# Kernel optimization log

Hardware: AMD Instinct MI355X
Metric: run time of the kernel (lower is better)

## Reference

```python
import jax, jax.numpy as jnp
import numpy as np

D_MODEL = 512
DFF = 2048
E = 8
K = 2
B, N = 2, 2048


def setup_inputs() -> dict:
    key = jax.random.key(0)
    ks = jax.random.split(key, 6)
    x = jax.random.normal(ks[0], (B, N, D_MODEL), dtype=jnp.float32)
    # router: nn.Linear(d_model, E, bias=False), init normal(std=0.01), weight [E, d]
    router_w = jax.random.normal(ks[1], (E, D_MODEL), dtype=jnp.float32) * 0.01
    # expert linear1.weight [dff, d], linear2.weight [d, dff], xavier-uniform; biases zero in torch init,
    # but use small random biases so the backward test exercises their grads meaningfully.
    lim1 = float(np.sqrt(6.0 / (D_MODEL + DFF)))
    w1_all = jax.random.uniform(ks[2], (E, DFF, D_MODEL), minval=-lim1, maxval=lim1, dtype=jnp.float32)
    w2_all = jax.random.uniform(ks[3], (E, D_MODEL, DFF), minval=-lim1, maxval=lim1, dtype=jnp.float32)
    b1_all = jax.random.normal(ks[4], (E, DFF), dtype=jnp.float32) * 0.01
    b2_all = jax.random.normal(ks[5], (E, D_MODEL), dtype=jnp.float32) * 0.01
    return {"x": x, "router_w": router_w, "w1_all": w1_all, "b1_all": b1_all,
            "w2_all": w2_all, "b2_all": b2_all}


def reference(x, router_w, w1_all, b1_all, w2_all, b2_all):
    Bb, Nn, C = x.shape
    L = Bb * Nn
    x_flat = x.reshape(L, C)

    # Router: logits -> softmax -> top-k -> renormalized weights
    router_logits = x_flat @ router_w.T                      # [L, E]
    router_probs = jax.nn.softmax(router_logits, axis=-1)
    expert_weights, expert_indices = jax.lax.top_k(router_probs, K)  # [L, K]
    expert_weights = expert_weights / (jnp.sum(expert_weights, axis=-1, keepdims=True) + 1e-9)

    # Dense per-expert MLP (same math as per-token gathered bmm; dropout in eval = identity)
    h = jax.nn.relu(jnp.einsum('lc,efc->lef', x_flat, w1_all) + b1_all[None])  # [L, E, dff]
    out_all = jnp.einsum('lef,ecf->lec', h, w2_all) + b2_all[None]             # [L, E, C]

    # Gather selected experts' outputs and combine
    out_sel = jnp.take_along_axis(out_all, expert_indices[:, :, None], axis=1)  # [L, K, C]
    final = jnp.sum(out_sel * expert_weights[:, :, None], axis=1)               # [L, C]
    return final.reshape(Bb, Nn, C)
```

## Files before the change

### kernel.cpp

```cpp
#include <hip/hip_runtime.h>

#define D_MODEL 512
#define DFF 2048
#define NEXP 8
#define LTOK 4096
#define NPAIR 8192
#define PMAX 9216
#define MAXT 72

#define HD_COUNTS 0
#define HD_CURSOR 8
#define HD_OFF    16
#define HD_NTILES 25
#define HD_TILE_E 32
#define HD_TILE_R 112

typedef __attribute__((ext_vector_type(8))) short bf16x8;
typedef __attribute__((ext_vector_type(4))) float f32x4;

__device__ __forceinline__ unsigned short f2bf(float f){
  unsigned u = __builtin_bit_cast(unsigned, f);
  u += 0x7fffu + ((u>>16)&1u);
  return (unsigned short)(u>>16);
}

__global__ void router_top2(const float* __restrict__ x, const float* __restrict__ rw,
                            int* __restrict__ pair_e, float* __restrict__ pair_w){
  int t = blockIdx.x;
  int l = threadIdx.x;
  const float* xr = x + (size_t)t*D_MODEL;
  float xv[8];
  #pragma unroll
  for (int j=0;j<8;j++) xv[j] = xr[j*64+l];
  double lg[NEXP];
  #pragma unroll
  for (int e=0;e<NEXP;e++){
    const float* we = rw + e*D_MODEL;
    double s = 0.0;
    #pragma unroll
    for (int j=0;j<8;j++) s += (double)xv[j] * (double)we[j*64+l];
    #pragma unroll
    for (int off=32; off; off>>=1) s += __shfl_xor(s, off);
    lg[e] = s;
  }
  if (l==0){
    double mx = lg[0];
    #pragma unroll
    for (int e=1;e<NEXP;e++) if (lg[e]>mx) mx = lg[e];
    double p[NEXP], sum = 0.0;
    #pragma unroll
    for (int e=0;e<NEXP;e++){ p[e] = exp(lg[e]-mx); sum += p[e]; }
    #pragma unroll
    for (int e=0;e<NEXP;e++) p[e] /= sum;
    int i0 = 0;
    for (int e=1;e<NEXP;e++) if (p[e] > p[i0]) i0 = e;
    int i1 = (i0==0) ? 1 : 0;
    for (int e=0;e<NEXP;e++){ if (e==i0) continue; if (p[e] > p[i1]) i1 = e; }
    double s2 = p[i0] + p[i1] + 1e-9;
    pair_e[2*t]   = i0;  pair_e[2*t+1] = i1;
    pair_w[2*t]   = (float)(p[i0]/s2);
    pair_w[2*t+1] = (float)(p[i1]/s2);
  }
}

__global__ void count_kernel(const int* __restrict__ pair_e, int* __restrict__ hdr){
  __shared__ int cnt[NEXP];
  int tid = threadIdx.x;
  if (tid < NEXP) cnt[tid] = 0;
  __syncthreads();
  int base = blockIdx.x*1024;
  #pragma unroll
  for (int i=0;i<4;i++) atomicAdd(&cnt[pair_e[base + i*256 + tid]], 1);
  __syncthreads();
  if (tid < NEXP) atomicAdd(&hdr[HD_COUNTS+tid], cnt[tid]);
}

__global__ void plan_kernel(int* __restrict__ hdr, int* __restrict__ gtok,
                            int* __restrict__ gtk){
  if (threadIdx.x==0){
    int off=0, nt=0;
    for (int e=0;e<NEXP;e++){
      hdr[HD_OFF+e]=off;
      int c = hdr[HD_COUNTS+e];
      int tiles = (c+127)>>7;
      for (int i=0;i<tiles;i++){ hdr[HD_TILE_E+nt]=e; hdr[HD_TILE_R+nt]=off+(i<<7); nt++; }
      off += tiles<<7;
    }
    hdr[HD_OFF+NEXP]=off;
    hdr[HD_NTILES]=nt;
  }
  for (int i=threadIdx.x; i<PMAX; i+=blockDim.x){ gtok[i]=0; gtk[i]=-1; }
}

__global__ void assign_kernel(const int* __restrict__ pair_e, int* __restrict__ hdr,
                              int* __restrict__ gtok, int* __restrict__ gtk){
  __shared__ int cnt[NEXP];
  __shared__ int base[NEXP];
  int tid = threadIdx.x;
  if (tid < NEXP) cnt[tid] = 0;
  __syncthreads();
  int id = blockIdx.x*256 + tid;
  int e = pair_e[id];
  int myrank = atomicAdd(&cnt[e], 1);
  __syncthreads();
  if (tid < NEXP) base[tid] = atomicAdd(&hdr[HD_CURSOR+tid], cnt[tid]);
  __syncthreads();
  int row = hdr[HD_OFF+e] + base[e] + myrank;
  gtok[row] = id>>1;
  gtk[row]  = id;
}

__global__ void gather_x_kernel(const float* __restrict__ x, const int* __restrict__ gtok,
                                unsigned short* __restrict__ xg){
  int id = blockIdx.x*256 + threadIdx.x;
  if (id >= PMAX*(D_MODEL/8)) return;
  int row = id>>6, j = id&63;
  int t = gtok[row];
  const float4* s = (const float4*)(x + (size_t)t*D_MODEL + j*8);
  float4 a = s[0], b = s[1];
  uint4 o;
  o.x = (unsigned)f2bf(a.x) | ((unsigned)f2bf(a.y)<<16);
  o.y = (unsigned)f2bf(a.z) | ((unsigned)f2bf(a.w)<<16);
  o.z = (unsigned)f2bf(b.x) | ((unsigned)f2bf(b.y)<<16);
  o.w = (unsigned)f2bf(b.z) | ((unsigned)f2bf(b.w)<<16);
  *(uint4*)(xg + (size_t)id*8) = o;
}

__global__ void convw_kernel(const float* __restrict__ w1, const float* __restrict__ w2,
                             unsigned short* __restrict__ w1b, unsigned short* __restrict__ w2b){
  int id = blockIdx.x*256 + threadIdx.x;
  const int per = NEXP*DFF*D_MODEL/8;
  const float* src; unsigned short* dst; int k;
  if (id < per){ src = w1; dst = w1b; k = id; }
  else         { src = w2; dst = w2b; k = id - per; }
  const float4* s = (const float4*)(src + (size_t)k*8);
  float4 a = s[0], b = s[1];
  uint4 o;
  o.x = (unsigned)f2bf(a.x) | ((unsigned)f2bf(a.y)<<16);
  o.y = (unsigned)f2bf(a.z) | ((unsigned)f2bf(a.w)<<16);
  o.z = (unsigned)f2bf(b.x) | ((unsigned)f2bf(b.y)<<16);
  o.w = (unsigned)f2bf(b.z) | ((unsigned)f2bf(b.w)<<16);
  *(uint4*)(dst + (size_t)k*8) = o;
}

template<int NDIM, int KDIM, int MODE>
__global__ __launch_bounds__(256,2) void gemm_moe(
    const unsigned short* __restrict__ A,
    const unsigned short* __restrict__ Bw,
    const float* __restrict__ bias,
    unsigned short* __restrict__ outH,
    float* __restrict__ outO,
    const float* __restrict__ pair_w,
    const int* __restrict__ hdr,
    const int* __restrict__ gtk)
{
  __shared__ __align__(16) unsigned short As[128*64];
  __shared__ __align__(16) unsigned short Bs[128*64];
  int bx = blockIdx.x;
  if (bx >= hdr[HD_NTILES]) return;
  int e    = hdr[HD_TILE_E+bx];
  int row0 = hdr[HD_TILE_R+bx];
  int n0   = blockIdx.y<<7;
  int tid  = threadIdx.x;
  int w = tid>>6, l = tid&63;
  int wm = w>>1, wn = w&1;

  const unsigned short* Ag = A  + (size_t)row0*KDIM;
  const unsigned short* Bg = Bw + (size_t)e*NDIM*KDIM + (size_t)n0*KDIM;

  f32x4 acc[4][4];
  f32x4 zz = {0.f,0.f,0.f,0.f};
  #pragma unroll
  for (int i=0;i<4;i++)
    #pragma unroll
    for (int j=0;j<4;j++) acc[i][j] = zz;

  int srow = (w<<3) + (l>>3);
  int c8   = l&7;
  char* AsB = (char*)As;
  char* BsB = (char*)Bs;

  for (int kt=0; kt<KDIM/64; ++kt){
    #pragma unroll
    for (int i=0;i<4;i++){
      int r  = i*32 + srow;
      int sc = (c8 ^ (r&7))*8;
      const unsigned short* ga = Ag + (size_t)r*KDIM + kt*64 + sc;
      const unsigned short* gb = Bg + (size_t)r*KDIM + kt*64 + sc;
      int ldso = i*4096 + w*1024 + l*16;
      __builtin_amdgcn_global_load_lds((const __attribute__((address_space(1))) void*)ga,
                                       (__attribute__((address_space(3))) void*)(AsB + ldso), 16, 0, 0);
      __builtin_amdgcn_global_load_lds((const __attribute__((address_space(1))) void*)gb,
                                       (__attribute__((address_space(3))) void*)(BsB + ldso), 16, 0, 0);
    }
    __syncthreads();
    #pragma unroll
    for (int kk=0;kk<2;kk++){
      bf16x8 av[4], bv[4];
      #pragma unroll
      for (int mi=0;mi<4;mi++){
        int r  = (wm<<6) + (mi<<4) + (l&15);
        int ch = ((kk<<2) + (l>>4)) ^ (r&7);
        av[mi] = *(const bf16x8*)(AsB + r*128 + ch*16);
      }
      #pragma unroll
      for (int ni=0;ni<4;ni++){
        int r  = (wn<<6) + (ni<<4) + (l&15);
        int ch = ((kk<<2) + (l>>4)) ^ (r&7);
        bv[ni] = *(const bf16x8*)(BsB + r*128 + ch*16);
      }
      #pragma unroll
      for (int mi=0;mi<4;mi++)
        #pragma unroll
        for (int ni=0;ni<4;ni++)
          acc[mi][ni] = __builtin_amdgcn_mfma_f32_16x16x32_bf16(av[mi], bv[ni], acc[mi][ni], 0,0,0);
    }
    __syncthreads();
  }

  int lc = l&15, lq = l>>4;
  #pragma unroll
  for (int ni=0;ni<4;ni++){
    int col = n0 + (wn<<6) + (ni<<4) + lc;
    float bcol = bias[e*NDIM + col];
    #pragma unroll
    for (int mi=0;mi<4;mi++){
      int rbase = row0 + (wm<<6) + (mi<<4) + lq*4;
      #pragma unroll
      for (int q=0;q<4;q++){
        int gr = rbase + q;
        float v = acc[mi][ni][q] + bcol;
        if (MODE==0){
          v = v>0.f ? v : 0.f;
          outH[(size_t)gr*NDIM + col] = f2bf(v);
        } else {
          int tk = gtk[gr];
          if (tk>=0){
            float wgt = pair_w[tk];
            atomicAdd(&outO[(size_t)(tk>>1)*D_MODEL + col], wgt*v);
          }
        }
      }
    }
  }
}

extern "C" void kernel_launch(void* const* d_in, const int* in_sizes, int n_in,
                              void* d_out, int out_size, void* d_ws, size_t ws_size,
                              hipStream_t stream){
  const float* x  = (const float*)d_in[0];
  const float* rw = (const float*)d_in[1];
  const float* w1 = (const float*)d_in[2];
  const float* b1 = (const float*)d_in[3];
  const float* w2 = (const float*)d_in[4];
  const float* b2 = (const float*)d_in[5];
  float* out = (float*)d_out;

  const size_t OFF_HDR  = 0;
  const size_t OFF_PE   = 1024;
  const size_t OFF_PW   = 66560;
  const size_t OFF_GTOK = 99328;
  const size_t OFF_GTK  = 136192;
  const size_t OFF_XG   = 180224;
  const size_t OFF_W1B  = OFF_XG  + (size_t)PMAX*D_MODEL*2;
  const size_t OFF_W2B  = OFF_W1B + (size_t)NEXP*DFF*D_MODEL*2;
  const size_t OFF_H    = OFF_W2B + (size_t)NEXP*DFF*D_MODEL*2;
  const size_t WS_NEED  = OFF_H   + (size_t)PMAX*DFF*2;
  if (ws_size < WS_NEED) return;

  char* ws = (char*)d_ws;
  int*   hdr    = (int*)(ws + OFF_HDR);
  int*   pair_e = (int*)(ws + OFF_PE);
  float* pair_w = (float*)(ws + OFF_PW);
  int*   gtok   = (int*)(ws + OFF_GTOK);
  int*   gtk    = (int*)(ws + OFF_GTK);
  unsigned short* xg  = (unsigned short*)(ws + OFF_XG);
  unsigned short* w1b = (unsigned short*)(ws + OFF_W1B);
  unsigned short* w2b = (unsigned short*)(ws + OFF_W2B);
  unsigned short* h   = (unsigned short*)(ws + OFF_H);

  hipMemsetAsync(hdr, 0, 1024, stream);
  hipMemsetAsync(out, 0, (size_t)LTOK*D_MODEL*sizeof(float), stream);
  router_top2<<<LTOK, 64, 0, stream>>>(x, rw, pair_e, pair_w);
  count_kernel<<<NPAIR/1024, 256, 0, stream>>>(pair_e, hdr);
  plan_kernel<<<1, 256, 0, stream>>>(hdr, gtok, gtk);
  assign_kernel<<<NPAIR/256, 256, 0, stream>>>(pair_e, hdr, gtok, gtk);
  gather_x_kernel<<<(PMAX*64)/256, 256, 0, stream>>>(x, gtok, xg);
  convw_kernel<<<8192, 256, 0, stream>>>(w1, w2, w1b, w2b);
  gemm_moe<DFF, D_MODEL, 0><<<dim3(MAXT,16), 256, 0, stream>>>(xg, w1b, b1, h, nullptr, nullptr, hdr, gtk);
  gemm_moe<D_MODEL, DFF, 1><<<dim3(MAXT,4), 256, 0, stream>>>(h, w2b, b2, nullptr, out, pair_w, hdr, gtk);
}
```

Before: 154.0 us.

## Fuse prep kernels and double-buffer both MoE GEMMs with retuned tiles

Merges weight conversion with the router, and merges token assignment with the x gather, which cuts kernel launches and the gtok buffer. Both expert GEMMs now use double-buffered LDS staging with async global-to-LDS loads, partial vmcnt waits and raw barriers, so loads overlap MFMA work. GEMM1 uses 128x256 tiles with 8 waves, GEMM2 uses 64x128 tiles with higher occupancy, and both use a workgroup swizzle for locality. The risks are correctness of the manual waitcnt and barrier handling, and padding rows of xg that are no longer zero-filled.

Result: no change. 156.8 us (+1.8%).

```diff
diff --git a/kernel.cpp b/kernel.cpp
--- a/kernel.cpp
+++ b/kernel.cpp
@@ -24,42 +24,68 @@
   return (unsigned short)(u>>16);
 }
 
-__global__ void router_top2(const float* __restrict__ x, const float* __restrict__ rw,
+template<int N> __device__ __forceinline__ void wait_vm(){
+  if constexpr (N==6)      asm volatile("s_waitcnt vmcnt(6)" ::: "memory");
+  else                     asm volatile("s_waitcnt vmcnt(0)" ::: "memory");
+}
+#define RAW_BARRIER() asm volatile("s_barrier" ::: "memory")
+
+__global__ void prep_kernel(const float* __restrict__ w1, const float* __restrict__ w2,
+                            unsigned short* __restrict__ w1b, unsigned short* __restrict__ w2b,
+                            const float* __restrict__ x, const float* __restrict__ rw,
                             int* __restrict__ pair_e, float* __restrict__ pair_w){
-  int t = blockIdx.x;
-  int l = threadIdx.x;
-  const float* xr = x + (size_t)t*D_MODEL;
-  float xv[8];
-  #pragma unroll
-  for (int j=0;j<8;j++) xv[j] = xr[j*64+l];
-  double lg[NEXP];
-  #pragma unroll
-  for (int e=0;e<NEXP;e++){
-    const float* we = rw + e*D_MODEL;
-    double s = 0.0;
-    #pragma unroll
-    for (int j=0;j<8;j++) s += (double)xv[j] * (double)we[j*64+l];
-    #pragma unroll
-    for (int off=32; off; off>>=1) s += __shfl_xor(s, off);
-    lg[e] = s;
-  }
-  if (l==0){
-    double mx = lg[0];
-    #pragma unroll
-    for (int e=1;e<NEXP;e++) if (lg[e]>mx) mx = lg[e];
-    double p[NEXP], sum = 0.0;
-    #pragma unroll
-    for (int e=0;e<NEXP;e++){ p[e] = exp(lg[e]-mx); sum += p[e]; }
-    #pragma unroll
-    for (int e=0;e<NEXP;e++) p[e] /= sum;
-    int i0 = 0;
-    for (int e=1;e<NEXP;e++) if (p[e] > p[i0]) i0 = e;
-    int i1 = (i0==0) ? 1 : 0;
-    for (int e=0;e<NEXP;e++){ if (e==i0) continue; if (p[e] > p[i1]) i1 = e; }
-    double s2 = p[i0] + p[i1] + 1e-9;
-    pair_e[2*t]   = i0;  pair_e[2*t+1] = i1;
-    pair_w[2*t]   = (float)(p[i0]/s2);
-    pair_w[2*t+1] = (float)(p[i1]/s2);
+  int bx = blockIdx.x;
+  int tid = threadIdx.x;
+  if (bx < 8192){
+    int id = bx*256 + tid;
+    const int per = NEXP*DFF*D_MODEL/8;
+    const float* src; unsigned short* dst; int k;
+    if (id < per){ src = w1; dst = w1b; k = id; }
+    else         { src = w2; dst = w2b; k = id - per; }
+    const float4* s = (const float4*)(src + (size_t)k*8);
+    float4 a = s[0], b = s[1];
+    uint4 o;
+    o.x = (unsigned)f2bf(a.x) | ((unsigned)f2bf(a.y)<<16);
+    o.y = (unsigned)f2bf(a.z) | ((unsigned)f2bf(a.w)<<16);
+    o.z = (unsigned)f2bf(b.x) | ((unsigned)f2bf(b.y)<<16);
+    o.w = (unsigned)f2bf(b.z) | ((unsigned)f2bf(b.w)<<16);
+    *(uint4*)(dst + (size_t)k*8) = o;
+  } else {
+    int t = (bx - 8192)*4 + (tid>>6);
+    int l = tid & 63;
+    const float* xr = x + (size_t)t*D_MODEL;
+    float xv[8];
+    #pragma unroll
+    for (int j=0;j<8;j++) xv[j] = xr[j*64+l];
+    double lg[NEXP];
+    #pragma unroll
+    for (int e=0;e<NEXP;e++){
+      const float* we = rw + e*D_MODEL;
+      double s = 0.0;
+      #pragma unroll
+      for (int j=0;j<8;j++) s += (double)xv[j] * (double)we[j*64+l];
+      #pragma unroll
+      for (int off=32; off; off>>=1) s += __shfl_xor(s, off);
+      lg[e] = s;
+    }
+    if (l==0){
+      double mx = lg[0];
+      #pragma unroll
+      for (int e=1;e<NEXP;e++) if (lg[e]>mx) mx = lg[e];
+      double p[NEXP], sum = 0.0;
+      #pragma unroll
+      for (int e=0;e<NEXP;e++){ p[e] = exp(lg[e]-mx); sum += p[e]; }
+      #pragma unroll
+      for (int e=0;e<NEXP;e++) p[e] /= sum;
+      int i0 = 0;
+      for (int e=1;e<NEXP;e++) if (p[e] > p[i0]) i0 = e;
+      int i1 = (i0==0) ? 1 : 0;
+      for (int e=0;e<NEXP;e++){ if (e==i0) continue; if (p[e] > p[i1]) i1 = e; }
+      double s2 = p[i0] + p[i1] + 1e-9;
+      pair_e[2*t]   = i0;  pair_e[2*t+1] = i1;
+      pair_w[2*t]   = (float)(p[i0]/s2);
+      pair_w[2*t+1] = (float)(p[i1]/s2);
+    }
   }
 }
 
@@ -75,8 +101,7 @@
   if (tid < NEXP) atomicAdd(&hdr[HD_COUNTS+tid], cnt[tid]);
 }
 
-__global__ void plan_kernel(int* __restrict__ hdr, int* __restrict__ gtok,
-                            int* __restrict__ gtk){
+__global__ void plan_kernel(int* __restrict__ hdr, int* __restrict__ gtk){
   if (threadIdx.x==0){
     int off=0, nt=0;
     for (int e=0;e<NEXP;e++){
@@ -89,13 +114,15 @@
     hdr[HD_OFF+NEXP]=off;
     hdr[HD_NTILES]=nt;
   }
-  for (int i=threadIdx.x; i<PMAX; i+=blockDim.x){ gtok[i]=0; gtk[i]=-1; }
-}
-
-__global__ void assign_kernel(const int* __restrict__ pair_e, int* __restrict__ hdr,
-                              int* __restrict__ gtok, int* __restrict__ gtk){
+  for (int i=threadIdx.x; i<PMAX; i+=blockDim.x) gtk[i]=-1;
+}
+
+__global__ void assign_gather_kernel(const int* __restrict__ pair_e, int* __restrict__ hdr,
+                                     int* __restrict__ gtk, const float* __restrict__ x,
+                                     unsigned short* __restrict__ xg){
   __shared__ int cnt[NEXP];
   __shared__ int base[NEXP];
+  __shared__ int rowbuf[256];
   int tid = threadIdx.x;
   if (tid < NEXP) cnt[tid] = 0;
   __syncthreads();
@@ -106,139 +133,258 @@
   if (tid < NEXP) base[tid] = atomicAdd(&hdr[HD_CURSOR+tid], cnt[tid]);
   __syncthreads();
   int row = hdr[HD_OFF+e] + base[e] + myrank;
-  gtok[row] = id>>1;
-  gtk[row]  = id;
-}
-
-__global__ void gather_x_kernel(const float* __restrict__ x, const int* __restrict__ gtok,
-                                unsigned short* __restrict__ xg){
-  int id = blockIdx.x*256 + threadIdx.x;
-  if (id >= PMAX*(D_MODEL/8)) return;
-  int row = id>>6, j = id&63;
-  int t = gtok[row];
-  const float4* s = (const float4*)(x + (size_t)t*D_MODEL + j*8);
-  float4 a = s[0], b = s[1];
-  uint4 o;
-  o.x = (unsigned)f2bf(a.x) | ((unsigned)f2bf(a.y)<<16);
-  o.y = (unsigned)f2bf(a.z) | ((unsigned)f2bf(a.w)<<16);
-  o.z = (unsigned)f2bf(b.x) | ((unsigned)f2bf(b.y)<<16);
-  o.w = (unsigned)f2bf(b.z) | ((unsigned)f2bf(b.w)<<16);
-  *(uint4*)(xg + (size_t)id*8) = o;
-}
-
-__global__ void convw_kernel(const float* __restrict__ w1, const float* __restrict__ w2,
-                             unsigned short* __restrict__ w1b, unsigned short* __restrict__ w2b){
-  int id = blockIdx.x*256 + threadIdx.x;
-  const int per = NEXP*DFF*D_MODEL/8;
-  const float* src; unsigned short* dst; int k;
-  if (id < per){ src = w1; dst = w1b; k = id; }
-  else         { src = w2; dst = w2b; k = id - per; }
-  const float4* s = (const float4*)(src + (size_t)k*8);
-  float4 a = s[0], b = s[1];
-  uint4 o;
-  o.x = (unsigned)f2bf(a.x) | ((unsigned)f2bf(a.y)<<16);
-  o.y = (unsigned)f2bf(a.z) | ((unsigned)f2bf(a.w)<<16);
-  o.z = (unsigned)f2bf(b.x) | ((unsigned)f2bf(b.y)<<16);
-  o.w = (unsigned)f2bf(b.z) | ((unsigned)f2bf(b.w)<<16);
-  *(uint4*)(dst + (size_t)k*8) = o;
-}
-
-template<int NDIM, int KDIM, int MODE>
-__global__ __launch_bounds__(256,2) void gemm_moe(
+  gtk[row] = id;
+  rowbuf[tid] = row;
+  __syncthreads();
+  int grp = tid>>6, sub = tid&63;
+  int base0 = blockIdx.x*256;
+  for (int p = grp; p < 256; p += 4){
+    int r = rowbuf[p];
+    int t = (base0 + p)>>1;
+    const float4* s = (const float4*)(x + (size_t)t*D_MODEL + sub*8);
+    float4 a = s[0], b = s[1];
+    uint4 o;
+    o.x = (unsigned)f2bf(a.x) | ((unsigned)f2bf(a.y)<<16);
+    o.y = (unsigned)f2bf(a.z) | ((unsigned)f2bf(a.w)<<16);
+    o.z = (unsigned)f2bf(b.x) | ((unsigned)f2bf(b.y)<<16);
+    o.w = (unsigned)f2bf(b.z) | ((unsigned)f2bf(b.w)<<16);
+    *(uint4*)(xg + (size_t)r*D_MODEL + sub*8) = o;
+  }
+}
+
+__global__ __launch_bounds__(512,2) void gemm1_k(
     const unsigned short* __restrict__ A,
     const unsigned short* __restrict__ Bw,
     const float* __restrict__ bias,
     unsigned short* __restrict__ outH,
+    const int* __restrict__ hdr)
+{
+  constexpr int NWG = MAXT*8;
+  __shared__ __align__(16) unsigned short As[2*128*64];
+  __shared__ __align__(16) unsigned short Bs[2*256*64];
+
+  int wg  = blockIdx.x;
+  int swz = (wg & 7)*(NWG/8) + (wg >> 3);
+  int m   = swz >> 3;
+  int n0  = (swz & 7) << 8;
+
+  if (m >= hdr[HD_NTILES]) return;
+  int e    = hdr[HD_TILE_E+m];
+  int row0 = hdr[HD_TILE_R+m];
+
+  int tid = threadIdx.x;
+  int w = tid>>6, l = tid&63;
+  int wm = w>>2, wn = w&3;
+
+  const unsigned short* Ag = A  + (size_t)row0*D_MODEL;
+  const unsigned short* Bg = Bw + (size_t)e*DFF*D_MODEL + (size_t)n0*D_MODEL;
+
+  f32x4 acc[4][4];
+  f32x4 zz = {0.f,0.f,0.f,0.f};
+  #pragma unroll
+  for (int i=0;i<4;i++)
+    #pragma unroll
+    for (int j=0;j<4;j++) acc[i][j] = zz;
+
+  int srow = (w<<3) + (l>>3);
+  int c8   = l&7;
+  char* AsB = (char*)As;
+  char* BsB = (char*)Bs;
+
+  auto stage = [&](int b, int kt){
+    #pragma unroll
+    for (int i=0;i<2;i++){
+      int r  = i*64 + srow;
+      int sc = (c8 ^ (r&7))*8;
+      const unsigned short* ga = Ag + (size_t)r*D_MODEL + kt*64 + sc;
+      int ldso = b*16384 + i*8192 + w*1024 + l*16;
+      __builtin_amdgcn_global_load_lds((const __attribute__((address_space(1))) void*)ga,
+                                       (__attribute__((address_space(3))) void*)(AsB + ldso), 16, 0, 0);
+    }
+    #pragma unroll
+    for (int i=0;i<4;i++){
+      int r  = i*64 + srow;
+      int sc = (c8 ^ (r&7))*8;
+      const unsigned short* gb = Bg + (size_t)r*D_MODEL + kt*64 + sc;
+      int ldso = b*32768 + i*8192 + w*1024 + l*16;
+      __builtin_amdgcn_global_load_lds((const __attribute__((address_space(1))) void*)gb,
+                                       (__attribute__((address_space(3))) void*)(BsB + ldso), 16, 0, 0);
+    }
+  };
+
+  auto compute = [&](int b){
+    #pragma unroll
+    for (int kk=0;kk<2;kk++){
+      bf16x8 av[4], bv[4];
+      #pragma unroll
+      for (int mi=0;mi<4;mi++){
+        int r  = (wm<<6) + (mi<<4) + (l&15);
+        int ch = ((kk<<2) + (l>>4)) ^ (r&7);
+        av[mi] = *(const bf16x8*)(AsB + b*16384 + r*128 + ch*16);
+      }
+      #pragma unroll
+      for (int ni=0;ni<4;ni++){
+        int r  = (wn<<6) + (ni<<4) + (l&15);
+        int ch = ((kk<<2) + (l>>4)) ^ (r&7);
+        bv[ni] = *(const bf16x8*)(BsB + b*32768 + r*128 + ch*16);
+      }
+      #pragma unroll
+      for (int mi=0;mi<4;mi++)
+        #pragma unroll
+        for (int ni=0;ni<4;ni++)
+          acc[mi][ni] = __builtin_amdgcn_mfma_f32_16x16x32_bf16(av[mi], bv[ni], acc[mi][ni], 0,0,0);
+    }
+  };
+
+  stage(0, 0);
+  int cur = 0;
+  for (int kt=0; kt<D_MODEL/64-1; ++kt){
+    stage(cur^1, kt+1);
+    wait_vm<6>();
+    RAW_BARRIER();
+    compute(cur);
+    asm volatile("s_waitcnt lgkmcnt(0)" ::: "memory");
+    RAW_BARRIER();
+    cur ^= 1;
+  }
+  wait_vm<0>();
+  RAW_BARRIER();
+  compute(cur);
+
+  int lc = l&15, lq = l>>4;
+  #pragma unroll
+  for (int ni=0;ni<4;ni++){
+    int col = n0 + (wn<<6) + (ni<<4) + lc;
+    float bcol = bias[e*DFF + col];
+    #pragma unroll
+    for (int mi=0;mi<4;mi++){
+      int rbase = row0 + (wm<<6) + (mi<<4) + lq*4;
+      #pragma unroll
+      for (int q=0;q<4;q++){
+        float v = acc[mi][ni][q] + bcol;
+        v = v>0.f ? v : 0.f;
+        outH[(size_t)(rbase+q)*DFF + col] = f2bf(v);
+      }
+    }
+  }
+}
+
+__global__ __launch_bounds__(256,3) void gemm2_k(
+    const unsigned short* __restrict__ A,
+    const unsigned short* __restrict__ Bw,
+    const float* __restrict__ bias,
     float* __restrict__ outO,
     const float* __restrict__ pair_w,
     const int* __restrict__ hdr,
     const int* __restrict__ gtk)
 {
-  __shared__ __align__(16) unsigned short As[128*64];
-  __shared__ __align__(16) unsigned short Bs[128*64];
-  int bx = blockIdx.x;
-  if (bx >= hdr[HD_NTILES]) return;
-  int e    = hdr[HD_TILE_E+bx];
-  int row0 = hdr[HD_TILE_R+bx];
-  int n0   = blockIdx.y<<7;
-  int tid  = threadIdx.x;
+  constexpr int NWG = 2*MAXT*4;
+  __shared__ __align__(16) unsigned short As[2*64*64];
+  __shared__ __align__(16) unsigned short Bs[2*128*64];
+
+  int wg  = blockIdx.x;
+  int swz = (wg & 7)*(NWG/8) + (wg >> 3);
+  int m   = swz >> 2;
+  int n0  = (swz & 3) << 7;
+
+  if (m >= 2*hdr[HD_NTILES]) return;
+  int e    = hdr[HD_TILE_E+(m>>1)];
+  int row0 = hdr[HD_TILE_R+(m>>1)] + ((m&1)<<6);
+
+  int tid = threadIdx.x;
   int w = tid>>6, l = tid&63;
-  int wm = w>>1, wn = w&1;
-
-  const unsigned short* Ag = A  + (size_t)row0*KDIM;
-  const unsigned short* Bg = Bw + (size_t)e*NDIM*KDIM + (size_t)n0*KDIM;
-
-  f32x4 acc[4][4];
+
+  const unsigned short* Ag = A  + (size_t)row0*DFF;
+  const unsigned short* Bg = Bw + (size_t)e*D_MODEL*DFF + (size_t)n0*DFF;
+
+  f32x4 acc[4][2];
   f32x4 zz = {0.f,0.f,0.f,0.f};
   #pragma unroll
   for (int i=0;i<4;i++)
     #pragma unroll
-    for (int j=0;j<4;j++) acc[i][j] = zz;
+    for (int j=0;j<2;j++) acc[i][j] = zz;
 
   int srow = (w<<3) + (l>>3);
   int c8   = l&7;
   char* AsB = (char*)As;
   char* BsB = (char*)Bs;
 
-  for (int kt=0; kt<KDIM/64; ++kt){
+  auto stage = [&](int b, int kt){
+    #pragma unroll
+    for (int i=0;i<2;i++){
+      int r  = i*32 + srow;
+      int sc = (c8 ^ (r&7))*8;
+      const unsigned short* ga = Ag + (size_t)r*DFF + kt*64 + sc;
+      int ldso = b*8192 + i*4096 + w*1024 + l*16;
+      __builtin_amdgcn_global_load_lds((const __attribute__((address_space(1))) void*)ga,
+                                       (__attribute__((address_space(3))) void*)(AsB + ldso), 16, 0, 0);
+    }
     #pragma unroll
     for (int i=0;i<4;i++){
       int r  = i*32 + srow;
       int sc = (c8 ^ (r&7))*8;
-      const unsigned short* ga = Ag + (size_t)r*KDIM + kt*64 + sc;
-      const unsigned short* gb = Bg + (size_t)r*KDIM + kt*64 + sc;
-      int ldso = i*4096 + w*1024 + l*16;
-      __builtin_amdgcn_global_load_lds((const __attribute__((address_space(1))) void*)ga,
-                                       (__attribute__((address_space(3))) void*)(AsB + ldso), 16, 0, 0);
+      const unsigned short* gb = Bg + (size_t)r*DFF + kt*64 + sc;
+      int ldso = b*16384 + i*4096 + w*1024 + l*16;
       __builtin_amdgcn_global_load_lds((const __attribute__((address_space(1))) void*)gb,
                                        (__attribute__((address_space(3))) void*)(BsB + ldso), 16, 0, 0);
     }
-    __syncthreads();
+  };
+
+  auto compute = [&](int b){
     #pragma unroll
     for (int kk=0;kk<2;kk++){
-      bf16x8 av[4], bv[4];
+      bf16x8 av[4], bv[2];
       #pragma unroll
       for (int mi=0;mi<4;mi++){
-        int r  = (wm<<6) + (mi<<4) + (l&15);
+        int r  = (mi<<4) + (l&15);
         int ch = ((kk<<2) + (l>>4)) ^ (r&7);
-        av[mi] = *(const bf16x8*)(AsB + r*128 + ch*16);
-      }
-      #pragma unroll
-      for (int ni=0;ni<4;ni++){
-        int r  = (wn<<6) + (ni<<4) + (l&15);
+        av[mi] = *(const bf16x8*)(AsB + b*8192 + r*128 + ch*16);
+      }
+      #pragma unroll
+      for (int ni=0;ni<2;ni++){
+        int r  = (w<<5) + (ni<<4) + (l&15);
         int ch = ((kk<<2) + (l>>4)) ^ (r&7);
-        bv[ni] = *(const bf16x8*)(BsB + r*128 + ch*16);
+        bv[ni] = *(const bf16x8*)(BsB + b*16384 + r*128 + ch*16);
       }
       #pragma unroll
       for (int mi=0;mi<4;mi++)
         #pragma unroll
-        for (int ni=0;ni<4;ni++)
+        for (int ni=0;ni<2;ni++)
           acc[mi][ni] = __builtin_amdgcn_mfma_f32_16x16x32_bf16(av[mi], bv[ni], acc[mi][ni], 0,0,0);
     }
-    __syncthreads();
-  }
+  };
+
+  stage(0, 0);
+  int cur = 0;
+  for (int kt=0; kt<DFF/64-1; ++kt){
+    stage(cur^1, kt+1);
+    wait_vm<6>();
+    RAW_BARRIER();
+    compute(cur);
+    asm volatile("s_waitcnt lgkmcnt(0)" ::: "memory");
+    RAW_BARRIER();
+    cur ^= 1;
+  }
+  wait_vm<0>();
+  RAW_BARRIER();
+  compute(cur);
 
   int lc = l&15, lq = l>>4;
   #pragma unroll
-  for (int ni=0;ni<4;ni++){
-    int col = n0 + (wn<<6) + (ni<<4) + lc;
-    float bcol = bias[e*NDIM + col];
+  for (int ni=0;ni<2;ni++){
+    int col = n0 + (w<<5) + (ni<<4) + lc;
+    float bcol = bias[e*D_MODEL + col];
     #pragma unroll
     for (int mi=0;mi<4;mi++){
-      int rbase = row0 + (wm<<6) + (mi<<4) + lq*4;
+      int rbase = row0 + (mi<<4) + lq*4;
       #pragma unroll
       for (int q=0;q<4;q++){
         int gr = rbase + q;
         float v = acc[mi][ni][q] + bcol;
-        if (MODE==0){
-          v = v>0.f ? v : 0.f;
-          outH[(size_t)gr*NDIM + col] = f2bf(v);
-        } else {
-          int tk = gtk[gr];
-          if (tk>=0){
-            float wgt = pair_w[tk];
-            atomicAdd(&outO[(size_t)(tk>>1)*D_MODEL + col], wgt*v);
-          }
+        int tk = gtk[gr];
+        if (tk>=0){
+          float wgt = pair_w[tk];
+          atomicAdd(&outO[(size_t)(tk>>1)*D_MODEL + col], wgt*v);
         }
       }
     }
@@ -259,8 +405,7 @@
   const size_t OFF_HDR  = 0;
   const size_t OFF_PE   = 1024;
   const size_t OFF_PW   = 66560;
-  const size_t OFF_GTOK = 99328;
-  const size_t OFF_GTK  = 136192;
+  const size_t OFF_GTK  = 99328;
   const size_t OFF_XG   = 180224;
   const size_t OFF_W1B  = OFF_XG  + (size_t)PMAX*D_MODEL*2;
   const size_t OFF_W2B  = OFF_W1B + (size_t)NEXP*DFF*D_MODEL*2;
@@ -272,7 +417,6 @@
   int*   hdr    = (int*)(ws + OFF_HDR);
   int*   pair_e = (int*)(ws + OFF_PE);
   float* pair_w = (float*)(ws + OFF_PW);
-  int*   gtok   = (int*)(ws + OFF_GTOK);
   int*   gtk    = (int*)(ws + OFF_GTK);
   unsigned short* xg  = (unsigned short*)(ws + OFF_XG);
   unsigned short* w1b = (unsigned short*)(ws + OFF_W1B);
@@ -281,12 +425,10 @@
 
   hipMemsetAsync(hdr, 0, 1024, stream);
   hipMemsetAsync(out, 0, (size_t)LTOK*D_MODEL*sizeof(float), stream);
-  router_top2<<<LTOK, 64, 0, stream>>>(x, rw, pair_e, pair_w);
+  prep_kernel<<<9216, 256, 0, stream>>>(w1, w2, w1b, w2b, x, rw, pair_e, pair_w);
   count_kernel<<<NPAIR/1024, 256, 0, stream>>>(pair_e, hdr);
-  plan_kernel<<<1, 256, 0, stream>>>(hdr, gtok, gtk);
-  assign_kernel<<<NPAIR/256, 256, 0, stream>>>(pair_e, hdr, gtok, gtk);
-  gather_x_kernel<<<(PMAX*64)/256, 256, 0, stream>>>(x, gtok, xg);
-  convw_kernel<<<8192, 256, 0, stream>>>(w1, w2, w1b, w2b);
-  gemm_moe<DFF, D_MODEL, 0><<<dim3(MAXT,16), 256, 0, stream>>>(xg, w1b, b1, h, nullptr, nullptr, hdr, gtk);
-  gemm_moe<D_MODEL, DFF, 1><<<dim3(MAXT,4), 256, 0, stream>>>(h, w2b, b2, nullptr, out, pair_w, hdr, gtk);
-}
+  plan_kernel<<<1, 256, 0, stream>>>(hdr, gtk);
+  assign_gather_kernel<<<NPAIR/256, 256, 0, stream>>>(pair_e, hdr, gtk, x, xg);
+  gemm1_k<<<MAXT*8, 512, 0, stream>>>(xg, w1b, b1, h, hdr);
+  gemm2_k<<<2*MAXT*4, 256, 0, stream>>>(h, w2b, b2, out, pair_w, hdr, gtk);
+}
```
